# Kernel optimization log

Hardware: AMD Instinct MI355X
Metric: run time of the kernel (lower is better)

## Reference

```python
import jax, jax.numpy as jnp
import numpy as np
import math

D_MODEL = 768
ED = 768           # d_inner = expand_factor * d_model = 768
N_STATE = 1        # ssm d_state
DT_RANK = math.ceil(D_MODEL / 16)  # 48
EPS = 1e-6


def setup_inputs() -> dict:
    key = jax.random.key(0)
    ks = jax.random.split(key, 12)
    s = lambda k, shape, scale: jax.random.normal(k, shape, dtype=jnp.float32) * scale
    x = jax.random.normal(ks[0], (8, 4096, D_MODEL), dtype=jnp.float32)
    return {
        "x": x,
        "rms_w": jnp.ones((D_MODEL,), jnp.float32),
        "in_proj_w": s(ks[1], (2 * ED, D_MODEL), 0.02),
        "conv_w": s(ks[2], (ED,), 0.5),          # depthwise conv, kernel=1 -> per-channel scale
        "conv_b": s(ks[3], (ED,), 0.02),
        "x_proj_w": s(ks[4], (DT_RANK + 2 * N_STATE, ED), 0.02),
        "dt_proj_w": s(ks[5], (ED, DT_RANK), 0.02),
        "dt_proj_b": s(ks[6], (ED,), 0.02),
        "A_log": jnp.log(jnp.tile(jnp.arange(1, N_STATE + 1, dtype=jnp.float32), (ED, 1))),  # (ED, N)
        "D": jnp.ones((ED,), jnp.float32),
        "out_proj_w": s(ks[7], (D_MODEL, ED), 0.02),
    }


def _selective_scan(xc, delta, A, Bm, C, D):
    # xc: (B,L,ED), delta: (B,L,ED), A: (ED,N), Bm: (B,L,N), C: (B,L,N)
    deltaA = jnp.exp(delta[..., None] * A)                      # (B,L,ED,N)
    deltaBx = delta[..., None] * Bm[:, :, None, :] * xc[..., None]  # (B,L,ED,N)

    def combine(left, right):
        a1, b1 = left
        a2, b2 = right
        return a1 * a2, a2 * b1 + b2

    _, hs = jax.lax.associative_scan(combine, (deltaA, deltaBx), axis=1)  # hs: (B,L,ED,N)
    y = jnp.einsum('blen,bln->ble', hs, C) + D * xc
    return y


def reference(x, rms_w, in_proj_w, conv_w, conv_b, x_proj_w, dt_proj_w,
              dt_proj_b, A_log, D, out_proj_w):
    # RMSNorm
    xn = x * jax.lax.rsqrt(jnp.mean(x * x, axis=-1, keepdims=True) + EPS) * rms_w

    # MambaBlock
    xz = xn @ in_proj_w.T                    # (B,L,2*ED)
    xc, z = jnp.split(xz, 2, axis=-1)
    # depthwise conv1d with kernel_size=1, padding=0 -> per-channel affine
    xc = jax.nn.silu(xc * conv_w + conv_b)

    dbc = xc @ x_proj_w.T                    # (B,L,dt_rank+2N)
    delta = dbc[..., :DT_RANK]
    Bm = dbc[..., DT_RANK:DT_RANK + N_STATE]
    C = dbc[..., DT_RANK + N_STATE:]
    delta = jax.nn.softplus(delta @ dt_proj_w.T + dt_proj_b)  # (B,L,ED)

    A = -jnp.exp(A_log)                      # (ED,N)
    y = _selective_scan(xc, delta, A, Bm, C, D)
    y = y * jax.nn.silu(z)
    return y @ out_proj_w.T                  # (B,L,D_MODEL)
```

## Files before the change

kernel.cpp:

```cpp
#include <hip/hip_runtime.h>

#define TOK   32768
#define DM    768
#define KDIM  768
#define LSEQ  4096
#define NC    64
#define CL    64
#define NCHAIN 6144

typedef __bf16 bf16x8 __attribute__((ext_vector_type(8)));
typedef float  f32x4  __attribute__((ext_vector_type(4)));
typedef unsigned short u16;
typedef unsigned int u32;

__device__ __forceinline__ u16 f2bf(float f) {
  unsigned u = __builtin_bit_cast(unsigned, f);
  u += 0x7fffu + ((u >> 16) & 1u);
  return (u16)(u >> 16);
}
__device__ __forceinline__ float bf2f(u32 h) {
  unsigned u = (h & 0xffffu) << 16;
  return __builtin_bit_cast(float, u);
}

#define GLOAD_LDS16(g, l) __builtin_amdgcn_global_load_lds( \
    (const __attribute__((address_space(1))) void*)(g),     \
    (__attribute__((address_space(3))) void*)(l), 16, 0, 0)

__global__ void cvt_k(const float* __restrict__ src, u16* __restrict__ dst, int n) {
  int i = blockIdx.x * 256 + threadIdx.x;
  if (i < n) dst[i] = f2bf(src[i]);
}

__global__ void cvt_pad_k(const float* __restrict__ src, u16* __restrict__ dst,
                          int rows, int cols, int dcols, int n) {
  int i = blockIdx.x * 256 + threadIdx.x;
  if (i >= n) return;
  int r = i / dcols, c = i % dcols;
  dst[i] = (r < rows && c < cols) ? f2bf(src[r * cols + c]) : (u16)0;
}

__global__ __launch_bounds__(192)
void rmsnorm_k(const float* __restrict__ x, const float* __restrict__ w,
               u16* __restrict__ xnb) {
  long t = blockIdx.x;
  int tid = threadIdx.x;
  float4 v = ((const float4*)x)[t * 192 + tid];
  float s = v.x * v.x + v.y * v.y + v.z * v.z + v.w * v.w;
#pragma unroll
  for (int o = 32; o; o >>= 1) s += __shfl_down(s, o, 64);
  __shared__ float red[3];
  if ((tid & 63) == 0) red[tid >> 6] = s;
  __syncthreads();
  float sc = rsqrtf((red[0] + red[1] + red[2]) * (1.f / 768.f) + 1e-6f);
  float4 ww = ((const float4*)w)[tid];
  ushort4 o;
  o.x = f2bf(v.x * sc * ww.x);
  o.y = f2bf(v.y * sc * ww.y);
  o.z = f2bf(v.z * sc * ww.z);
  o.w = f2bf(v.w * sc * ww.w);
  ((ushort4*)xnb)[t * 192 + tid] = o;
}

template <int EPI>
__global__ __launch_bounds__(256)
void gemm32(const u16* __restrict__ A, int lda,
            const u16* __restrict__ B, int ldb, int K,
            int GX, int RPX,
            float* __restrict__ C,
            const float* __restrict__ w0, const float* __restrict__ w1,
            u16* __restrict__ o0, u16* __restrict__ o1) {
  __shared__ __align__(16) u16 smA[3 * 4096];
  __shared__ __align__(16) u16 smB[3 * 4096];
  const int tid = threadIdx.x;
  const int lane = tid & 63;
  const int wid = tid >> 6;

  const int bid = blockIdx.x;
  const int xcd = bid & 7;
  const int p = bid >> 3;
  const int colp = p % GX;
  const int rowp = xcd * RPX + p / GX;
  const long rowBase = (long)rowp * 128;
  const long colBase = (long)colp * 128;

  const int wr = (wid >> 1) * 64;
  const int wc = (wid & 1) * 64;
  const int lr = lane & 15;
  const int kc = lane >> 4;
  const int kcs = kc ^ ((lr >> 1) & 3);

  const int c1 = tid + 256;
  const u16* gA0 = A + (rowBase + (tid >> 2)) * lda + ((tid & 3) ^ ((tid >> 3) & 3)) * 8;
  const u16* gA1 = A + (rowBase + (c1 >> 2)) * lda + ((c1 & 3) ^ ((c1 >> 3) & 3)) * 8;
  const u16* gB0 = B + (colBase + (tid >> 2)) * ldb + ((tid & 3) ^ ((tid >> 3) & 3)) * 8;
  const u16* gB1 = B + (colBase + (c1 >> 2)) * ldb + ((c1 & 3) ^ ((c1 >> 3) & 3)) * 8;

  f32x4 acc[4][4] = {};
  const int NT = K >> 5;

  auto STAGE = [&](int buf, int kt) {
    u16* bA = smA + buf * 4096;
    u16* bB = smB + buf * 4096;
    GLOAD_LDS16(gA0 + kt, &bA[tid * 8]);
    GLOAD_LDS16(gA1 + kt, &bA[c1 * 8]);
    GLOAD_LDS16(gB0 + kt, &bB[tid * 8]);
    GLOAD_LDS16(gB1 + kt, &bB[c1 * 8]);
  };

  STAGE(0, 0);
  STAGE(1, 32);
  asm volatile("s_waitcnt vmcnt(4)" ::: "memory");
  __builtin_amdgcn_s_barrier();

  for (int t = 0; t < NT; ++t) {
    const u16* cA = smA + (t % 3) * 4096;
    const u16* cB = smB + (t % 3) * 4096;
    bf16x8 af[4], bfr[4];
#pragma unroll
    for (int m = 0; m < 4; ++m)
      af[m] = *(const bf16x8*)&cA[(wr + m * 16 + lr) * 32 + kcs * 8];
#pragma unroll
    for (int n = 0; n < 4; ++n)
      bfr[n] = *(const bf16x8*)&cB[(wc + n * 16 + lr) * 32 + kcs * 8];
    if (t + 2 < NT) STAGE((t + 2) % 3, (t + 2) << 5);
#pragma unroll
    for (int m = 0; m < 4; ++m)
#pragma unroll
      for (int n = 0; n < 4; ++n)
        acc[m][n] = __builtin_amdgcn_mfma_f32_16x16x32_bf16(af[m], bfr[n], acc[m][n], 0, 0, 0);
    if (t + 1 < NT) {
      if (t + 2 < NT) asm volatile("s_waitcnt vmcnt(4) lgkmcnt(0)" ::: "memory");
      else            asm volatile("s_waitcnt vmcnt(0) lgkmcnt(0)" ::: "memory");
      __builtin_amdgcn_s_barrier();
    }
  }

#pragma unroll
  for (int m = 0; m < 4; ++m)
#pragma unroll
    for (int n = 0; n < 4; ++n)
#pragma unroll
      for (int j = 0; j < 4; ++j) {
        long grow = rowBase + wr + m * 16 + kc * 4 + j;
        long gcol = colBase + wc + n * 16 + lr;
        float v = acc[m][n][j];
        if (EPI == 0) {
          C[grow * DM + gcol] = v;
        } else if (EPI == 1) {
          if (gcol < DM) {
            float t = v * w0[gcol] + w1[gcol];
            o0[grow * DM + gcol] = f2bf(t / (1.f + __expf(-t)));
          } else {
            o1[grow * DM + (gcol - DM)] = f2bf(v / (1.f + __expf(-v)));
          }
        } else if (EPI == 2) {
          float t = v + w0[gcol];
          float d = (t > 20.f) ? t : __logf(1.f + __expf(t));
          o0[grow * DM + gcol] = f2bf(d);
        } else {
          if (gcol < 64) o0[grow * 64 + gcol] = f2bf(v);
          if (gcol == 48) C[grow * 2 + 0] = v;
          if (gcol == 49) C[grow * 2 + 1] = v;
        }
      }
}

__global__ __launch_bounds__(384)
void scan1_k(const u16* __restrict__ deltab, const u16* __restrict__ xcb,
             const float* __restrict__ bmc, const float* __restrict__ A_log,
             float* __restrict__ aprod, float* __restrict__ hend) {
  int pe = threadIdx.x;
  int b = blockIdx.x, c = blockIdx.y;
  int e0 = pe * 2;
  float Ae0 = -__expf(A_log[e0]), Ae1 = -__expf(A_log[e0 + 1]);
  float ap0 = 1.f, h0 = 0.f, ap1 = 1.f, h1 = 0.f;
  long base = (long)b * LSEQ + (long)c * CL;
  for (int i = 0; i < CL; ++i) {
    long t = base + i;
    u32 dv = *(const u32*)&deltab[t * DM + e0];
    u32 xv = *(const u32*)&xcb[t * DM + e0];
    float Bm = bmc[t * 2];
    float d0 = bf2f(dv), d1 = bf2f(dv >> 16);
    float x0 = bf2f(xv), x1 = bf2f(xv >> 16);
    float a0 = __expf(d0 * Ae0), a1 = __expf(d1 * Ae1);
    ap0 *= a0; h0 = a0 * h0 + d0 * Bm * x0;
    ap1 *= a1; h1 = a1 * h1 + d1 * Bm * x1;
  }
  long chain = (long)c * NCHAIN + b * DM + e0;
  *(float2*)&aprod[chain] = make_float2(ap0, ap1);
  *(float2*)&hend[chain]  = make_float2(h0, h1);
}

__global__ __launch_bounds__(256)
void scan2_k(const float* __restrict__ aprod, const float* __restrict__ hend,
             float* __restrict__ carry) {
  int chain = blockIdx.x * 256 + threadIdx.x;
  float h = 0.f;
  for (int c = 0; c < NC; ++c) {
    carry[c * NCHAIN + chain] = h;
    h = aprod[c * NCHAIN + chain] * h + hend[c * NCHAIN + chain];
  }
}

__global__ __launch_bounds__(384)
void scan3_k(const u16* __restrict__ deltab, const u16* __restrict__ xcb,
             const float* __restrict__ bmc, const float* __restrict__ A_log,
             const float* __restrict__ Dp, const u16* __restrict__ szb,
             const float* __restrict__ carry, u16* __restrict__ ybf) {
  int pe = threadIdx.x;
  int b = blockIdx.x, c = blockIdx.y;
  int e0 = pe * 2;
  float Ae0 = -__expf(A_log[e0]), Ae1 = -__expf(A_log[e0 + 1]);
  float De0 = Dp[e0], De1 = Dp[e0 + 1];
  long chain = (long)c * NCHAIN + b * DM + e0;
  float2 hc = *(const float2*)&carry[chain];
  float h0 = hc.x, h1 = hc.y;
  long base = (long)b * LSEQ + (long)c * CL;
  for (int i = 0; i < CL; ++i) {
    long t = base + i;
    u32 dv = *(const u32*)&deltab[t * DM + e0];
    u32 xv = *(const u32*)&xcb[t * DM + e0];
    u32 sv = *(const u32*)&szb[t * DM + e0];
    float Bm = bmc[t * 2], Cc = bmc[t * 2 + 1];
    float d0 = bf2f(dv), d1 = bf2f(dv >> 16);
    float x0 = bf2f(xv), x1 = bf2f(xv >> 16);
    float a0 = __expf(d0 * Ae0), a1 = __expf(d1 * Ae1);
    h0 = a0 * h0 + d0 * Bm * x0;
    h1 = a1 * h1 + d1 * Bm * x1;
    float y0 = (h0 * Cc + De0 * x0) * bf2f(sv);
    float y1 = (h1 * Cc + De1 * x1) * bf2f(sv >> 16);
    *(u32*)&ybf[t * DM + e0] = (u32)f2bf(y0) | ((u32)f2bf(y1) << 16);
  }
}

extern "C" void kernel_launch(void* const* d_in, const int* in_sizes, int n_in,
                              void* d_out, int out_size, void* d_ws, size_t ws_size,
                              hipStream_t stream) {
  const float* x         = (const float*)d_in[0];
  const float* rms_w     = (const float*)d_in[1];
  const float* in_proj_w = (const float*)d_in[2];
  const float* conv_w    = (const float*)d_in[3];
  const float* conv_b    = (const float*)d_in[4];
  const float* x_proj_w  = (const float*)d_in[5];
  const float* dt_proj_w = (const float*)d_in[6];
  const float* dt_proj_b = (const float*)d_in[7];
  const float* A_log     = (const float*)d_in[8];
  const float* Dp        = (const float*)d_in[9];
  const float* out_proj_w= (const float*)d_in[10];
  float* out = (float*)d_out;

  char* ws = (char*)d_ws;
  size_t off = 0;
  auto alloc = [&](size_t bytes) -> void* {
    void* p = ws + off;
    off += (bytes + 255) & ~(size_t)255;
    return p;
  };
  u16*   xnb    = (u16*)alloc((size_t)TOK * DM * 2);
  u16*   xcb    = (u16*)alloc((size_t)TOK * DM * 2);
  u16*   szb    = (u16*)alloc((size_t)TOK * DM * 2);
  u16*   ybf    = (u16*)alloc((size_t)TOK * DM * 2);
  u16*   deltab = (u16*)alloc((size_t)TOK * DM * 2);
  u16*   dbcb   = (u16*)alloc((size_t)TOK * 64 * 2);
  float* bmc    = (float*)alloc((size_t)TOK * 2 * 4);
  u16*   wInB   = (u16*)alloc((size_t)1536 * 768 * 2);
  u16*   wXpB   = (u16*)alloc((size_t)128 * 768 * 2);
  u16*   wDtB   = (u16*)alloc((size_t)768 * 64 * 2);
  u16*   wOutB  = (u16*)alloc((size_t)768 * 768 * 2);
  float* aprod  = (float*)alloc((size_t)NC * NCHAIN * 4);
  float* hend   = (float*)alloc((size_t)NC * NCHAIN * 4);
  float* carry  = (float*)alloc((size_t)NC * NCHAIN * 4);

  cvt_k<<<(1536 * 768 + 255) / 256, 256, 0, stream>>>(in_proj_w, wInB, 1536 * 768);
  cvt_k<<<(768 * 768 + 255) / 256, 256, 0, stream>>>(out_proj_w, wOutB, 768 * 768);
  cvt_pad_k<<<(128 * 768 + 255) / 256, 256, 0, stream>>>(x_proj_w, wXpB, 50, 768, 768, 128 * 768);
  cvt_pad_k<<<(768 * 64 + 255) / 256, 256, 0, stream>>>(dt_proj_w, wDtB, 768, 48, 64, 768 * 64);

  rmsnorm_k<<<TOK, 192, 0, stream>>>(x, rms_w, xnb);

  gemm32<1><<<3072, 256, 0, stream>>>(
      xnb, DM, wInB, DM, KDIM, 12, 32, nullptr, conv_w, conv_b, xcb, szb);

  gemm32<3><<<256, 256, 0, stream>>>(
      xcb, DM, wXpB, DM, KDIM, 1, 32, bmc, nullptr, nullptr, dbcb, nullptr);

  gemm32<2><<<1536, 256, 0, stream>>>(
      dbcb, 64, wDtB, 64, 64, 6, 32, nullptr, dt_proj_b, nullptr, deltab, nullptr);

  scan1_k<<<dim3(8, NC), 384, 0, stream>>>(deltab, xcb, bmc, A_log, aprod, hend);
  scan2_k<<<NCHAIN / 256, 256, 0, stream>>>(aprod, hend, carry);
  scan3_k<<<dim3(8, NC), 384, 0, stream>>>(deltab, xcb, bmc, A_log, Dp, szb, carry, ybf);

  gemm32<0><<<1536, 256, 0, stream>>>(
      ybf, DM, wOutB, DM, KDIM, 6, 32, out, nullptr, nullptr, nullptr, nullptr);
}
```

Before: 328.9 us.

## Load GEMM A operand directly from global into registers, bypassing LDS

The A tile is no longer staged through shared memory. Each wave now reads its A fragments straight from global memory into registers, double-buffered across k-steps, while B keeps the three-stage LDS pipeline. This halves the LDS footprint and the LDS read traffic, and may allow higher occupancy. In exchange, the two waves that share the same rows both fetch the same A data from global/L2, and the 16-byte row-strided loads are less coalesced than the old cooperative staging. The wait counts were also adjusted for the extra outstanding loads, which is fragile.

```diff
diff --git a/kernel.cpp b/kernel.cpp
--- a/kernel.cpp
+++ b/kernel.cpp
@@ -70,7 +70,6 @@
             float* __restrict__ C,
             const float* __restrict__ w0, const float* __restrict__ w1,
             u16* __restrict__ o0, u16* __restrict__ o1) {
-  __shared__ __align__(16) u16 smA[3 * 4096];
   __shared__ __align__(16) u16 smB[3 * 4096];
   const int tid = threadIdx.x;
   const int lane = tid & 63;
@@ -91,48 +90,76 @@
   const int kcs = kc ^ ((lr >> 1) & 3);
 
   const int c1 = tid + 256;
-  const u16* gA0 = A + (rowBase + (tid >> 2)) * lda + ((tid & 3) ^ ((tid >> 3) & 3)) * 8;
-  const u16* gA1 = A + (rowBase + (c1 >> 2)) * lda + ((c1 & 3) ^ ((c1 >> 3) & 3)) * 8;
   const u16* gB0 = B + (colBase + (tid >> 2)) * ldb + ((tid & 3) ^ ((tid >> 3) & 3)) * 8;
   const u16* gB1 = B + (colBase + (c1 >> 2)) * ldb + ((c1 & 3) ^ ((c1 >> 3) & 3)) * 8;
 
+  const u16* aR[4];
+#pragma unroll
+  for (int m = 0; m < 4; ++m)
+    aR[m] = A + (rowBase + wr + m * 16 + lr) * lda + kc * 8;
+
   f32x4 acc[4][4] = {};
   const int NT = K >> 5;
 
-  auto STAGE = [&](int buf, int kt) {
-    u16* bA = smA + buf * 4096;
+  auto STAGE_B = [&](int buf, int kt) {
     u16* bB = smB + buf * 4096;
-    GLOAD_LDS16(gA0 + kt, &bA[tid * 8]);
-    GLOAD_LDS16(gA1 + kt, &bA[c1 * 8]);
     GLOAD_LDS16(gB0 + kt, &bB[tid * 8]);
     GLOAD_LDS16(gB1 + kt, &bB[c1 * 8]);
   };
 
-  STAGE(0, 0);
-  STAGE(1, 32);
-  asm volatile("s_waitcnt vmcnt(4)" ::: "memory");
+  bf16x8 afA[4], afB[4];
+
+  STAGE_B(0, 0);
+  STAGE_B(1, 32);
+#pragma unroll
+  for (int m = 0; m < 4; ++m) afA[m] = *(const bf16x8*)(aR[m]);
+  asm volatile("s_waitcnt vmcnt(0)" ::: "memory");
   __builtin_amdgcn_s_barrier();
 
-  for (int t = 0; t < NT; ++t) {
-    const u16* cA = smA + (t % 3) * 4096;
-    const u16* cB = smB + (t % 3) * 4096;
-    bf16x8 af[4], bfr[4];
-#pragma unroll
-    for (int m = 0; m < 4; ++m)
-      af[m] = *(const bf16x8*)&cA[(wr + m * 16 + lr) * 32 + kcs * 8];
-#pragma unroll
-    for (int n = 0; n < 4; ++n)
-      bfr[n] = *(const bf16x8*)&cB[(wc + n * 16 + lr) * 32 + kcs * 8];
-    if (t + 2 < NT) STAGE((t + 2) % 3, (t + 2) << 5);
-#pragma unroll
-    for (int m = 0; m < 4; ++m)
+  for (int tt = 0; tt < NT; tt += 2) {
+    {
+      const int t = tt;
+      const u16* cB = smB + (t % 3) * 4096;
+      bf16x8 bfr[4];
 #pragma unroll
       for (int n = 0; n < 4; ++n)
-        acc[m][n] = __builtin_amdgcn_mfma_f32_16x16x32_bf16(af[m], bfr[n], acc[m][n], 0, 0, 0);
-    if (t + 1 < NT) {
-      if (t + 2 < NT) asm volatile("s_waitcnt vmcnt(4) lgkmcnt(0)" ::: "memory");
-      else            asm volatile("s_waitcnt vmcnt(0) lgkmcnt(0)" ::: "memory");
+        bfr[n] = *(const bf16x8*)&cB[(wc + n * 16 + lr) * 32 + kcs * 8];
+      if (t + 2 < NT) STAGE_B((t + 2) % 3, (t + 2) << 5);
+#pragma unroll
+      for (int m = 0; m < 4; ++m)
+        afB[m] = *(const bf16x8*)(aR[m] + ((t + 1) << 5));
+#pragma unroll
+      for (int m = 0; m < 4; ++m)
+#pragma unroll
+        for (int n = 0; n < 4; ++n)
+          acc[m][n] = __builtin_amdgcn_mfma_f32_16x16x32_bf16(afA[m], bfr[n], acc[m][n], 0, 0, 0);
+      if (t + 2 < NT) asm volatile("s_waitcnt vmcnt(6)" ::: "memory");
+      else            asm volatile("s_waitcnt vmcnt(4)" ::: "memory");
       __builtin_amdgcn_s_barrier();
+    }
+    {
+      const int t = tt + 1;
+      const u16* cB = smB + (t % 3) * 4096;
+      bf16x8 bfr[4];
+#pragma unroll
+      for (int n = 0; n < 4; ++n)
+        bfr[n] = *(const bf16x8*)&cB[(wc + n * 16 + lr) * 32 + kcs * 8];
+      if (t + 2 < NT) STAGE_B((t + 2) % 3, (t + 2) << 5);
+      if (t + 1 < NT) {
+#pragma unroll
+        for (int m = 0; m < 4; ++m)
+          afA[m] = *(const bf16x8*)(aR[m] + ((t + 1) << 5));
+      }
+#pragma unroll
+      for (int m = 0; m < 4; ++m)
+#pragma unroll
+        for (int n = 0; n < 4; ++n)
+          acc[m][n] = __builtin_amdgcn_mfma_f32_16x16x32_bf16(afB[m], bfr[n], acc[m][n], 0, 0, 0);
+      if (t + 1 < NT) {
+        if (t + 2 < NT) asm volatile("s_waitcnt vmcnt(6)" ::: "memory");
+        else            asm volatile("s_waitcnt vmcnt(4)" ::: "memory");
+        __builtin_amdgcn_s_barrier();
+      }
     }
   }
 
```

Measured after the change: 489.8 us. 48.9% more time.

## Use 256x128 tiles with 512-thread blocks for in_proj and out_proj GEMMs

Applied to the files above, without the earlier changes.

Adds a gemm512 kernel that uses 8 waves per block to compute a 256x128 output tile with double-buffered LDS, replacing the 128x128, 3-stage gemm32 for the input and output projections. The larger tile reuses each B tile across more rows and halves the block count. It drops from triple to double buffering and puts a full barrier on every K step, so less global-load latency can be hidden. gemm32 is trimmed to the remaining epilogues.

```diff
diff --git a/kernel.cpp b/kernel.cpp
--- a/kernel.cpp
+++ b/kernel.cpp
@@ -63,13 +63,101 @@
 }
 
 template <int EPI>
+__global__ __launch_bounds__(512)
+void gemm512(const u16* __restrict__ A, int lda,
+             const u16* __restrict__ B, int ldb, int K,
+             int GX, int RPX,
+             float* __restrict__ C,
+             const float* __restrict__ w0, const float* __restrict__ w1,
+             u16* __restrict__ o0, u16* __restrict__ o1) {
+  __shared__ __align__(16) u16 smA[2 * 8192];
+  __shared__ __align__(16) u16 smB[2 * 4096];
+  const int tid = threadIdx.x;
+  const int lane = tid & 63;
+  const int wid = tid >> 6;
+
+  const int bid = blockIdx.x;
+  const int xcd = bid & 7;
+  const int p = bid >> 3;
+  const int colp = p % GX;
+  const int rowp = xcd * RPX + p / GX;
+  const long rowBase = (long)rowp * 256;
+  const long colBase = (long)colp * 128;
+
+  const int wr = (wid >> 1) * 64;
+  const int wc = (wid & 1) * 64;
+  const int lr = lane & 15;
+  const int kc = lane >> 4;
+  const int kcs = kc ^ ((lr >> 1) & 3);
+
+  const int c1 = tid + 512;
+  const u16* gA0 = A + (rowBase + (tid >> 2)) * lda + ((tid & 3) ^ ((tid >> 3) & 3)) * 8;
+  const u16* gA1 = A + (rowBase + (c1 >> 2)) * lda + ((c1 & 3) ^ ((c1 >> 3) & 3)) * 8;
+  const u16* gB0 = B + (colBase + (tid >> 2)) * ldb + ((tid & 3) ^ ((tid >> 3) & 3)) * 8;
+
+  f32x4 acc[4][4] = {};
+  const int NT = K >> 5;
+
+  auto STAGE = [&](int buf, int kt) {
+    u16* bA = smA + buf * 8192;
+    u16* bB = smB + buf * 4096;
+    GLOAD_LDS16(gA0 + kt, &bA[tid * 8]);
+    GLOAD_LDS16(gA1 + kt, &bA[c1 * 8]);
+    GLOAD_LDS16(gB0 + kt, &bB[tid * 8]);
+  };
+
+  STAGE(0, 0);
+  __syncthreads();
+
+  for (int t = 0; t < NT; ++t) {
+    if (t + 1 < NT) STAGE((t + 1) & 1, (t + 1) << 5);
+    const u16* cA = smA + (t & 1) * 8192;
+    const u16* cB = smB + (t & 1) * 4096;
+    bf16x8 af[4], bfr[4];
+#pragma unroll
+    for (int m = 0; m < 4; ++m)
+      af[m] = *(const bf16x8*)&cA[(wr + m * 16 + lr) * 32 + kcs * 8];
+#pragma unroll
+    for (int n = 0; n < 4; ++n)
+      bfr[n] = *(const bf16x8*)&cB[(wc + n * 16 + lr) * 32 + kcs * 8];
+#pragma unroll
+    for (int m = 0; m < 4; ++m)
+#pragma unroll
+      for (int n = 0; n < 4; ++n)
+        acc[m][n] = __builtin_amdgcn_mfma_f32_16x16x32_bf16(af[m], bfr[n], acc[m][n], 0, 0, 0);
+    __syncthreads();
+  }
+
+#pragma unroll
+  for (int m = 0; m < 4; ++m)
+#pragma unroll
+    for (int n = 0; n < 4; ++n)
+#pragma unroll
+      for (int j = 0; j < 4; ++j) {
+        long grow = rowBase + wr + m * 16 + kc * 4 + j;
+        long gcol = colBase + wc + n * 16 + lr;
+        float v = acc[m][n][j];
+        if (EPI == 0) {
+          C[grow * DM + gcol] = v;
+        } else {
+          if (gcol < DM) {
+            float t = v * w0[gcol] + w1[gcol];
+            o0[grow * DM + gcol] = f2bf(t / (1.f + __expf(-t)));
+          } else {
+            o1[grow * DM + (gcol - DM)] = f2bf(v / (1.f + __expf(-v)));
+          }
+        }
+      }
+}
+
+template <int EPI>
 __global__ __launch_bounds__(256)
 void gemm32(const u16* __restrict__ A, int lda,
             const u16* __restrict__ B, int ldb, int K,
             int GX, int RPX,
             float* __restrict__ C,
-            const float* __restrict__ w0, const float* __restrict__ w1,
-            u16* __restrict__ o0, u16* __restrict__ o1) {
+            const float* __restrict__ w0,
+            u16* __restrict__ o0) {
   __shared__ __align__(16) u16 smA[3 * 4096];
   __shared__ __align__(16) u16 smB[3 * 4096];
   const int tid = threadIdx.x;
@@ -145,16 +233,7 @@
         long grow = rowBase + wr + m * 16 + kc * 4 + j;
         long gcol = colBase + wc + n * 16 + lr;
         float v = acc[m][n][j];
-        if (EPI == 0) {
-          C[grow * DM + gcol] = v;
-        } else if (EPI == 1) {
-          if (gcol < DM) {
-            float t = v * w0[gcol] + w1[gcol];
-            o0[grow * DM + gcol] = f2bf(t / (1.f + __expf(-t)));
-          } else {
-            o1[grow * DM + (gcol - DM)] = f2bf(v / (1.f + __expf(-v)));
-          }
-        } else if (EPI == 2) {
+        if (EPI == 2) {
           float t = v + w0[gcol];
           float d = (t > 20.f) ? t : __logf(1.f + __expf(t));
           o0[grow * DM + gcol] = f2bf(d);
@@ -279,19 +358,19 @@
 
   rmsnorm_k<<<TOK, 192, 0, stream>>>(x, rms_w, xnb);
 
-  gemm32<1><<<3072, 256, 0, stream>>>(
-      xnb, DM, wInB, DM, KDIM, 12, 32, nullptr, conv_w, conv_b, xcb, szb);
+  gemm512<1><<<1536, 512, 0, stream>>>(
+      xnb, DM, wInB, DM, KDIM, 12, 16, nullptr, conv_w, conv_b, xcb, szb);
 
   gemm32<3><<<256, 256, 0, stream>>>(
-      xcb, DM, wXpB, DM, KDIM, 1, 32, bmc, nullptr, nullptr, dbcb, nullptr);
+      xcb, DM, wXpB, DM, KDIM, 1, 32, bmc, nullptr, dbcb);
 
   gemm32<2><<<1536, 256, 0, stream>>>(
-      dbcb, 64, wDtB, 64, 64, 6, 32, nullptr, dt_proj_b, nullptr, deltab, nullptr);
+      dbcb, 64, wDtB, 64, 64, 6, 32, nullptr, dt_proj_b, deltab);
 
   scan1_k<<<dim3(8, NC), 384, 0, stream>>>(deltab, xcb, bmc, A_log, aprod, hend);
   scan2_k<<<NCHAIN / 256, 256, 0, stream>>>(aprod, hend, carry);
   scan3_k<<<dim3(8, NC), 384, 0, stream>>>(deltab, xcb, bmc, A_log, Dp, szb, carry, ybf);
 
-  gemm32<0><<<1536, 256, 0, stream>>>(
-      ybf, DM, wOutB, DM, KDIM, 6, 32, out, nullptr, nullptr, nullptr, nullptr);
-}
+  gemm512<0><<<768, 512, 0, stream>>>(
+      ybf, DM, wOutB, DM, KDIM, 6, 16, out, nullptr, nullptr, nullptr, nullptr);
+}
```

Measured after the change: 331.3 us. About the same (+0.7%).
